# Optimization experiments

Measured on AMD Instinct MI355X. Metric: run time of the kernel, lower is better.

Reference implementation:

```python
import jax, jax.numpy as jnp
import numpy as np

B, T, S, E, H = 64, 256, 512, 128, 512


def setup_inputs() -> dict:
    key = jax.random.key(0)
    ks = jax.random.split(key, 18)
    sc = 0.02
    return {
        "trg_embed": jax.random.normal(ks[0], (B, T, E), jnp.float32),
        "encoder_hidden": jax.random.normal(ks[1], (B, S, 2 * H), jnp.float32),
        "encoder_final_h": jax.random.normal(ks[2], (1, B, 2 * H), jnp.float32),
        "encoder_final_c": jax.random.normal(ks[3], (1, B, 2 * H), jnp.float32),
        "src_mask": jnp.ones((B, 1, S), jnp.bool_),
        "trg_mask": jnp.ones((B, 1, T), jnp.bool_),
        "W_key": jax.random.normal(ks[4], (H, 2 * H), jnp.float32) * sc,
        "W_query": jax.random.normal(ks[5], (H, H), jnp.float32) * sc,
        "v_att": jax.random.normal(ks[6], (H,), jnp.float32) * sc,
        "bridgeh_w": jax.random.normal(ks[7], (H, 2 * H), jnp.float32) * sc,
        "bridgeh_b": jax.random.normal(ks[8], (H,), jnp.float32) * sc,
        "bridgec_w": jax.random.normal(ks[9], (H, 2 * H), jnp.float32) * sc,
        "bridgec_b": jax.random.normal(ks[10], (H,), jnp.float32) * sc,
        "W_ih": jax.random.normal(ks[11], (4 * H, E + 2 * H), jnp.float32) * sc,
        "W_hh": jax.random.normal(ks[12], (4 * H, H), jnp.float32) * sc,
        "b_ih": jax.random.normal(ks[13], (4 * H,), jnp.float32) * sc,
        "b_hh": jax.random.normal(ks[14], (4 * H,), jnp.float32) * sc,
        "W_pre": jax.random.normal(ks[15], (H, H + 2 * H + E), jnp.float32) * sc,
    }


def reference(trg_embed, encoder_hidden, encoder_final_h, encoder_final_c,
              src_mask, trg_mask, W_key, W_query, v_att,
              bridgeh_w, bridgeh_b, bridgec_w, bridgec_b,
              W_ih, W_hh, b_ih, b_hh, W_pre):
    # bridge: init hidden/cell from encoder final states (num_layers=1)
    h = jnp.tanh(encoder_final_h[0] @ bridgeh_w.T + bridgeh_b)  # [B,H]
    c = jnp.tanh(encoder_final_c[0] @ bridgec_w.T + bridgec_b)  # [B,H]

    # Bahdanau attention: precompute key projection once
    proj_key = jnp.einsum('bsk,hk->bsh', encoder_hidden, W_key)  # [B,S,H]
    mask = src_mask[:, 0, :]  # [B,S]
    neg = jnp.asarray(-1e9, encoder_hidden.dtype)

    def step(carry, x_t):
        h, c = carry  # [B,H] each; x_t: [B,E]
        q = h @ W_query.T  # query = last-layer hidden, [B,H]
        scores = jnp.einsum('bsh,h->bs', jnp.tanh(proj_key + q[:, None, :]), v_att)
        scores = jnp.where(mask, scores, neg)
        alphas = jax.nn.softmax(scores, axis=-1)
        ctx = jnp.einsum('bs,bsk->bk', alphas, encoder_hidden)  # [B,2H]
        x = jnp.concatenate([x_t, ctx], axis=-1)  # [B,E+2H]
        gates = x @ W_ih.T + h @ W_hh.T + (b_ih + b_hh)  # [B,4H]
        i, f, g, o = jnp.split(gates, 4, axis=-1)  # torch LSTM gate order
        c_new = jax.nn.sigmoid(f) * c + jax.nn.sigmoid(i) * jnp.tanh(g)
        h_new = jax.nn.sigmoid(o) * jnp.tanh(c_new)
        return (h_new, c_new), (h_new, ctx)

    (h, c), (outs, ctxs) = jax.lax.scan(step, (h, c), jnp.swapaxes(trg_embed, 0, 1))
    outs = jnp.swapaxes(outs, 0, 1)  # decoder_states [B,T,H]
    ctxs = jnp.swapaxes(ctxs, 0, 1)  # [B,T,2H]
    # pre_output projection (dropout p=0 -> identity), batched over all steps
    pre = jnp.concatenate([trg_embed, outs, ctxs], axis=-1) @ W_pre.T  # [B,T,H]
    return outs, h[None], c[None], pre
```

## Files before the change

kernel.cpp:

```cpp
#include <hip/hip_runtime.h>

#define Tq 256
#define Sq 512
#define Hq 512
#define H2q 1024
#define KPACK 1664

typedef __attribute__((ext_vector_type(8))) short short8_t;
typedef __attribute__((ext_vector_type(4))) float f32x4;

__device__ __forceinline__ float bf2f(ushort u){ return __uint_as_float(((unsigned)u)<<16); }
__device__ __forceinline__ ushort f2bf(float f){
  unsigned u = __float_as_uint(f);
  u += 0x7FFFu + ((u>>16)&1u);
  return (ushort)(u>>16);
}
__device__ __forceinline__ float frcp(float x){ return __builtin_amdgcn_rcpf(x); }
__device__ __forceinline__ float fexp2(float x){ return __builtin_amdgcn_exp2f(x); }
__device__ __forceinline__ float ftanh(float x){
  return 1.f - 2.f*frcp(fexp2(2.8853900818f*x) + 1.f);
}
__device__ __forceinline__ float fsig(float x){
  return frcp(1.f + fexp2(-1.4426950409f*x));
}

__global__ void bail_kernel(float* out, float v){
  if (threadIdx.x < 256) out[threadIdx.x] = v;
}

__global__ void conv_bf16(const float* __restrict__ src, ushort* __restrict__ dst, int n4){
  int idx = blockIdx.x*blockDim.x + threadIdx.x;
  if (idx >= n4) return;
  float4 v = ((const float4*)src)[idx];
  ushort4 o; o.x = f2bf(v.x); o.y = f2bf(v.y); o.z = f2bf(v.z); o.w = f2bf(v.w);
  ((ushort4*)dst)[idx] = o;
}

__global__ void conv_fp8(const float* __restrict__ src, unsigned* __restrict__ dst, int n4){
  int idx = blockIdx.x*blockDim.x + threadIdx.x;
  if (idx >= n4) return;
  float4 v = ((const float4*)src)[idx];
  unsigned u = __builtin_amdgcn_cvt_pk_fp8_f32(v.x, v.y, 0u, false);
  u = __builtin_amdgcn_cvt_pk_fp8_f32(v.z, v.w, u, true);
  dst[idx] = u;
}

__global__ void pack_trg(const float* __restrict__ trg, ushort* __restrict__ packed, int n4){
  int idx = blockIdx.x*blockDim.x + threadIdx.x;
  if (idx >= n4) return;
  float4 v = ((const float4*)trg)[idx];
  int bt = idx >> 5, r = idx & 31;
  ushort4 o; o.x = f2bf(v.x); o.y = f2bf(v.y); o.z = f2bf(v.z); o.w = f2bf(v.w);
  *(ushort4*)&packed[(long)bt*KPACK + r*4] = o;
}

__global__ void bsum_kernel(const float* __restrict__ a, const float* __restrict__ b,
                            float* __restrict__ o, int n){
  int idx = blockIdx.x*blockDim.x + threadIdx.x;
  if (idx < n) o[idx] = a[idx] + b[idx];
}

__global__ __launch_bounds__(512)
void bridge_kernel(const float* __restrict__ efh, const float* __restrict__ efc,
                   const float* __restrict__ bhw, const float* __restrict__ bhb,
                   const float* __restrict__ bcw, const float* __restrict__ bcb,
                   float* __restrict__ hb0, float* __restrict__ cws)
{
  int b = blockIdx.x, n = threadIdx.x;
  __shared__ __align__(16) float eh_l[1024];
  __shared__ __align__(16) float ec_l[1024];
  eh_l[n]       = efh[b*1024 + n];
  eh_l[n + 512] = efh[b*1024 + 512 + n];
  ec_l[n]       = efc[b*1024 + n];
  ec_l[n + 512] = efc[b*1024 + 512 + n];
  __syncthreads();
  const float4* wh = (const float4*)(bhw + (long)n*1024);
  const float4* wc = (const float4*)(bcw + (long)n*1024);
  float ah = bhb[n], ac = bcb[n];
  for (int i = 0; i < 256; ++i) {
    float4 w1 = wh[i]; float4 w2 = wc[i];
    const float* e1 = &eh_l[i*4]; const float* e2 = &ec_l[i*4];
    ah += w1.x*e1[0] + w1.y*e1[1] + w1.z*e1[2] + w1.w*e1[3];
    ac += w2.x*e2[0] + w2.y*e2[1] + w2.z*e2[2] + w2.w*e2[3];
  }
  hb0[b*512 + n] = ftanh(ah);
  cws[b*512 + n] = ftanh(ac);
}

__global__ __launch_bounds__(256)
void gemm_bt(const ushort* __restrict__ A, int lda, long sA,
             const ushort* __restrict__ Bt, int ldb, long sB,
             void* __restrict__ Cout, int ldc, long sC, int K, int outMode)
{
  __shared__ __align__(16) ushort Al[128][40];
  __shared__ __align__(16) ushort Bl[128][40];
  int bz = blockIdx.z;
  const ushort* Ab = A + (long)bz*sA;
  const ushort* Bb = Bt + (long)bz*sB;
  int m0 = blockIdx.x*128, n0 = blockIdx.y*128;
  int tid = threadIdx.x;
  int lane = tid & 63, w = tid >> 6;
  int wm = w >> 1, wn = w & 1;
  f32x4 acc[4][4] = {};
  int frow = lane & 15, fk = (lane >> 4)*8;
  for (int k0 = 0; k0 < K; k0 += 32) {
    #pragma unroll
    for (int p = 0; p < 2; ++p) {
      int task = tid + p*256;
      int row = task >> 2, c8 = (task & 3)*8;
      uint4 va = *(const uint4*)(Ab + (long)(m0+row)*lda + k0 + c8);
      uint4 vb = *(const uint4*)(Bb + (long)(n0+row)*ldb + k0 + c8);
      *(uint4*)&Al[row][c8] = va;
      *(uint4*)&Bl[row][c8] = vb;
    }
    __syncthreads();
    short8_t af[4], bfr[4];
    #pragma unroll
    for (int mi = 0; mi < 4; ++mi) af[mi]  = *(const short8_t*)&Al[wm*64 + mi*16 + frow][fk];
    #pragma unroll
    for (int ni = 0; ni < 4; ++ni) bfr[ni] = *(const short8_t*)&Bl[wn*64 + ni*16 + frow][fk];
    #pragma unroll
    for (int mi = 0; mi < 4; ++mi)
      #pragma unroll
      for (int ni = 0; ni < 4; ++ni)
        acc[mi][ni] = __builtin_amdgcn_mfma_f32_16x16x32_bf16(af[mi], bfr[ni], acc[mi][ni], 0, 0, 0);
    __syncthreads();
  }
  int rbase = (lane >> 4)*4;
  int col = lane & 15;
  #pragma unroll
  for (int mi = 0; mi < 4; ++mi)
    #pragma unroll
    for (int ni = 0; ni < 4; ++ni)
      #pragma unroll
      for (int i = 0; i < 4; ++i) {
        int gm = m0 + wm*64 + mi*16 + rbase + i;
        int gn = n0 + wn*64 + ni*16 + col;
        float vv = acc[mi][ni][i];
        long off = (long)bz*sC + (long)gm*ldc + gn;
        if (outMode == 1)      ((ushort*)Cout)[off] = f2bf(vv);
        else if (outMode == 2) ((unsigned char*)Cout)[off] =
              (unsigned char)(__builtin_amdgcn_cvt_pk_fp8_f32(vv, 0.f, 0, false) & 0xFF);
        else                   ((float*)Cout)[off] = vv;
      }
}

__global__ __launch_bounds__(512)
void qstep(const ushort* __restrict__ Wq, const float* __restrict__ hr,
           float* __restrict__ qbuf)
{
  __shared__ __align__(16) float h_s[512];
  int b = blockIdx.x, tid = threadIdx.x;
  h_s[tid] = hr[b*Hq + tid];
  __syncthreads();
  const ushort* wrow = Wq + (long)tid*Hq;
  float qa = 0.f;
  #pragma unroll 4
  for (int k = 0; k < 512; k += 8) {
    uint4 w4 = *(const uint4*)(wrow + k);
    const ushort* wu = (const ushort*)&w4;
    #pragma unroll
    for (int e = 0; e < 8; ++e) qa += h_s[k+e]*bf2f(wu[e]);
  }
  qbuf[b*Hq + tid] = qa;
}

__global__ __launch_bounds__(512)
void scoreA(const unsigned char* __restrict__ pk8,
            const unsigned char* __restrict__ eh8,
            const ushort* __restrict__ qpart,
            const float* __restrict__ qbuf,
            const float* __restrict__ vatt,
            float* __restrict__ ctxp,
            float* __restrict__ denp,
            int useQbuf)
{
  __shared__ __align__(16) float q_s[512];
  __shared__ __align__(16) float v_s[512];
  __shared__ __align__(16) float sred[512];
  __shared__ __align__(16) float e_s[64];
  int tid = threadIdx.x, blk = blockIdx.x;
  int b = blk >> 3, j8 = blk & 7, s0 = j8*64;
  if (useQbuf) {
    q_s[tid] = qbuf[b*Hq + tid];
  } else {
    const ushort* qp = qpart + (long)b*32*512 + tid;
    float qa = 0.f;
    #pragma unroll 8
    for (int c = 0; c < 32; ++c) qa += bf2f(qp[c*512]);
    q_s[tid] = qa;
  }
  v_s[tid] = vatt[tid];
  __syncthreads();
  int sl = tid & 63, hq = tid >> 6;
  {
    const unsigned char* pr = pk8 + ((long)b*Sq + s0 + sl)*Hq + hq*64;
    float p = 0.f;
    #pragma unroll
    for (int i = 0; i < 4; ++i) {
      uint4 w4 = *(const uint4*)(pr + i*16);
      const unsigned* uw = (const unsigned*)&w4;
      #pragma unroll
      for (int m = 0; m < 4; ++m) {
        unsigned u = uw[m];
        int hb = hq*64 + i*16 + m*4;
        p += v_s[hb+0]*ftanh(__builtin_amdgcn_cvt_f32_fp8(u,0) + q_s[hb+0]);
        p += v_s[hb+1]*ftanh(__builtin_amdgcn_cvt_f32_fp8(u,1) + q_s[hb+1]);
        p += v_s[hb+2]*ftanh(__builtin_amdgcn_cvt_f32_fp8(u,2) + q_s[hb+2]);
        p += v_s[hb+3]*ftanh(__builtin_amdgcn_cvt_f32_fp8(u,3) + q_s[hb+3]);
      }
    }
    sred[hq*64 + sl] = p;
  }
  __syncthreads();
  if (tid < 64) {
    float sc = 0.f;
    #pragma unroll
    for (int g = 0; g < 8; ++g) sc += sred[g*64 + tid];
    float e = fexp2(1.4426950409f*sc);
    e_s[tid] = e;
    float r = e;
    #pragma unroll
    for (int off = 32; off; off >>= 1) r += __shfl_down(r, off);
    if (tid == 0) denp[b*8 + j8] = r;
  }
  __syncthreads();
  {
    const unsigned char* ep = eh8 + ((long)b*Sq + s0)*H2q + tid*2;
    float a0 = 0.f, a1 = 0.f;
    #pragma unroll 4
    for (int s = 0; s < 64; ++s) {
      unsigned u = (unsigned)(*(const ushort*)(ep + (long)s*H2q));
      float es = e_s[s];
      a0 += es*__builtin_amdgcn_cvt_f32_fp8(u,0);
      a1 += es*__builtin_amdgcn_cvt_f32_fp8(u,1);
    }
    float* cp = ctxp + ((long)b*8 + j8)*1024 + tid*2;
    cp[0] = a0; cp[1] = a1;
  }
}

__global__ __launch_bounds__(512)
void gatesB(int t, ushort* packed,
            const ushort* __restrict__ Wih, const ushort* __restrict__ Whh,
            const ushort* __restrict__ Wq,
            const float* __restrict__ bsum, const float* __restrict__ hr,
            float* __restrict__ hw, float* __restrict__ cws,
            const float* __restrict__ ctxp, const float* __restrict__ denp,
            ushort* __restrict__ qpart,
            float* __restrict__ outs)
{
  __shared__ __align__(16) float x_lds[8*KPACK];
  __shared__ __align__(16) float g_lds[512];
  __shared__ __align__(16) float rden[8];
  __shared__ __align__(16) float hn_s[128];
  float* redc = x_lds;
  int tid = threadIdx.x, blk = blockIdx.x;
  int c_bg = blk >> 5, c_rc = blk & 31;

  if (tid < 8) {
    int gb = c_bg*8 + tid;
    float d = 0.f;
    #pragma unroll
    for (int j = 0; j < 8; ++j) d += denp[gb*8 + j];
    rden[tid] = frcp(d);
  }
  for (int task = tid; task < 128; task += 512) {
    int bb = task >> 4, c8 = task & 15;
    int gb = c_bg*8 + bb;
    uint4 vv = *(const uint4*)(packed + (long)(gb*Tq + t)*KPACK + c8*8);
    const ushort* uu = (const ushort*)&vv;
    #pragma unroll
    for (int e = 0; e < 8; ++e) x_lds[bb*KPACK + c8*8 + e] = bf2f(uu[e]);
  }
  for (int task = tid; task < 4096; task += 512) {
    int bb = task >> 9, kk = task & 511;
    x_lds[bb*KPACK + 1152 + kk] = hr[(c_bg*8 + bb)*Hq + kk];
  }
  __syncthreads();
  for (int task = tid; task < 8192; task += 512) {
    int bb = task >> 10, kk = task & 1023;
    int gb = c_bg*8 + bb;
    const float* cp = ctxp + (long)gb*8*1024 + kk;
    float cv = 0.f;
    #pragma unroll
    for (int j = 0; j < 8; ++j) cv += cp[j*1024];
    cv *= rden[bb];
    x_lds[bb*KPACK + 128 + kk] = cv;
    if (c_rc == 0) packed[(long)(gb*Tq + t)*KPACK + 640 + kk] = f2bf(cv);
  }
  __syncthreads();
  float acc0[8] = {}, acc1[8] = {};
  int rt = tid & 31, ks = tid >> 5;
  int rowslot0 = rt*2;
  int rr0 = (rowslot0 >> 4)*512 + c_rc*16 + (rowslot0 & 15);
  for (int kt = 0; kt < 13; ++kt) {
    const ushort* w0 = (kt < 9) ? (Wih + (long)rr0*1152 + kt*128 + ks*8)
                                : (Whh + (long)rr0*512  + (kt-9)*128 + ks*8);
    const ushort* w1 = w0 + ((kt < 9) ? 1152 : 512);
    uint4 wa = *(const uint4*)w0;
    uint4 wb = *(const uint4*)w1;
    const ushort* wua = (const ushort*)&wa;
    const ushort* wub = (const ushort*)&wb;
    float wf0[8], wf1[8];
    #pragma unroll
    for (int e = 0; e < 8; ++e) { wf0[e] = bf2f(wua[e]); wf1[e] = bf2f(wub[e]); }
    int xbase = kt*128 + ks*8;
    #pragma unroll
    for (int bb = 0; bb < 8; ++bb) {
      const float* xp = &x_lds[bb*KPACK + xbase];
      float4 x0 = *(const float4*)xp;
      float4 x1 = *(const float4*)(xp + 4);
      acc0[bb] += wf0[0]*x0.x + wf0[1]*x0.y + wf0[2]*x0.z + wf0[3]*x0.w
                + wf0[4]*x1.x + wf0[5]*x1.y + wf0[6]*x1.z + wf0[7]*x1.w;
      acc1[bb] += wf1[0]*x0.x + wf1[1]*x0.y + wf1[2]*x0.z + wf1[3]*x0.w
                + wf1[4]*x1.x + wf1[5]*x1.y + wf1[6]*x1.z + wf1[7]*x1.w;
    }
  }
  __syncthreads();
  #pragma unroll
  for (int bb = 0; bb < 8; ++bb) {
    redc[bb*1024 + ks*64 + rowslot0]     = acc0[bb];
    redc[bb*1024 + ks*64 + rowslot0 + 1] = acc1[bb];
  }
  __syncthreads();
  {
    int rowslot = tid & 63, bb = tid >> 6;
    float gvv = bsum[(rowslot >> 4)*512 + c_rc*16 + (rowslot & 15)];
    #pragma unroll
    for (int q2 = 0; q2 < 16; ++q2) gvv += redc[bb*1024 + q2*64 + rowslot];
    g_lds[bb*64 + rowslot] = gvv;
  }
  __syncthreads();
  if (tid < 128) {
    int bb = tid >> 4, i2 = tid & 15;
    int gb = c_bg*8 + bb;
    int hd = c_rc*16 + i2;
    float gi = g_lds[bb*64 +  0 + i2];
    float gf = g_lds[bb*64 + 16 + i2];
    float gg = g_lds[bb*64 + 32 + i2];
    float go = g_lds[bb*64 + 48 + i2];
    float co = cws[gb*Hq + hd];
    float cn = fsig(gf)*co + fsig(gi)*ftanh(gg);
    float hn = fsig(go)*ftanh(cn);
    cws[gb*Hq + hd] = cn;
    hw[gb*Hq + hd] = hn;
    outs[(long)(gb*Tq + t)*Hq + hd] = hn;
    packed[(long)(gb*Tq + t)*KPACK + 128 + hd] = f2bf(hn);
    hn_s[bb*16 + i2] = hn;
  }
  __syncthreads();
  {
    const ushort* wr = Wq + (long)tid*Hq + c_rc*16;
    uint4 wa = *(const uint4*)wr;
    uint4 wb = *(const uint4*)(wr + 8);
    const ushort* wua = (const ushort*)&wa;
    const ushort* wub = (const ushort*)&wb;
    float wf[16];
    #pragma unroll
    for (int e = 0; e < 8; ++e) { wf[e] = bf2f(wua[e]); wf[8+e] = bf2f(wub[e]); }
    #pragma unroll
    for (int bb = 0; bb < 8; ++bb) {
      const float* hp = &hn_s[bb*16];
      float qa = 0.f;
      #pragma unroll
      for (int e = 0; e < 16; ++e) qa += wf[e]*hp[e];
      qpart[((long)(c_bg*8 + bb)*32 + c_rc)*512 + tid] = f2bf(qa);
    }
  }
}

__global__ void epilogue_copy(const float* __restrict__ hb0, const float* __restrict__ cws,
                              float* __restrict__ dout){
  int idx = blockIdx.x*blockDim.x + threadIdx.x;
  if (idx < 32768) {
    dout[8388608 + idx] = hb0[idx];
    dout[8421376 + idx] = cws[idx];
  }
}

extern "C" void kernel_launch(void* const* d_in, const int* in_sizes, int n_in,
                              void* d_out, int out_size, void* d_ws, size_t ws_size,
                              hipStream_t stream)
{
  float* out = (float*)d_out;
  static const int expect[18] = {2097152,33554432,65536,65536,32768,16384,
                                 524288,262144,512,524288,512,524288,512,
                                 2359296,1048576,2048,2048,851968};
  if (n_in != 18 || out_size != 16842752) {
    bail_kernel<<<1, 256, 0, stream>>>(out, 33.0f); return;
  }
  for (int i = 0; i < 18; ++i) if (in_sizes[i] != expect[i]) {
    bail_kernel<<<1, 256, 0, stream>>>(out, 100.0f + i); return;
  }
  if (ws_size < 166207552ULL) { bail_kernel<<<1, 256, 0, stream>>>(out, 77.0f); return; }

  const float* trg  = (const float*)d_in[0];
  const float* eh   = (const float*)d_in[1];
  const float* efh  = (const float*)d_in[2];
  const float* efc  = (const float*)d_in[3];
  const float* Wk   = (const float*)d_in[6];
  const float* Wq   = (const float*)d_in[7];
  const float* v    = (const float*)d_in[8];
  const float* bhw  = (const float*)d_in[9];
  const float* bhb  = (const float*)d_in[10];
  const float* bcw  = (const float*)d_in[11];
  const float* bcb  = (const float*)d_in[12];
  const float* Wih  = (const float*)d_in[13];
  const float* Whh  = (const float*)d_in[14];
  const float* bih  = (const float*)d_in[15];
  const float* bhh  = (const float*)d_in[16];
  const float* Wpre = (const float*)d_in[17];
  char* ws = (char*)d_ws;

  ushort* ehb          = (ushort*)(ws + 0);
  unsigned char* eh8   = (unsigned char*)(ws + 0);
  unsigned char* pk8   = (unsigned char*)(ws + 67108864);
  ushort* packed       = (ushort*)(ws + 83886080);
  ushort* Wk_b         = (ushort*)(ws + 138412032);
  ushort* Wq_b         = (ushort*)(ws + 139460608);
  ushort* Wih_b        = (ushort*)(ws + 139984896);
  ushort* Whh_b        = (ushort*)(ws + 144703488);
  ushort* Wpre_b       = (ushort*)(ws + 146800640);
  float*  qbuf         = (float*)(ws + 148504576);
  float*  ctxp         = (float*)(ws + 148635648);
  float*  denp         = (float*)(ws + 150732800);
  float*  bsum         = (float*)(ws + 150734848);
  float*  hb0          = (float*)(ws + 150743040);
  float*  hb1          = (float*)(ws + 150874112);
  float*  cws          = (float*)(ws + 151005184);
  ushort* qpart        = (ushort*)(ws + 151136256);

  auto cb = [&](const float* s, ushort* d, int n){
    int n4 = n/4;
    conv_bf16<<<(n4 + 255)/256, 256, 0, stream>>>(s, d, n4);
  };
  cb(eh,   ehb,   64*512*1024);
  cb(Wk,   Wk_b,  512*1024);
  cb(Wq,   Wq_b,  512*512);
  cb(Wih,  Wih_b, 2048*1152);
  cb(Whh,  Whh_b, 2048*512);
  cb(Wpre, Wpre_b,512*1664);
  pack_trg<<<(524288 + 255)/256, 256, 0, stream>>>(trg, packed, 524288);
  bsum_kernel<<<8, 256, 0, stream>>>(bih, bhh, bsum, 2048);
  bridge_kernel<<<64, 512, 0, stream>>>(efh, efc, bhw, bhb, bcw, bcb, hb0, cws);
  gemm_bt<<<dim3(4,4,64), 256, 0, stream>>>(ehb, 1024, 524288L, Wk_b, 1024, 0L,
                                            (void*)pk8, 512, 262144L, 1024, 2);
  conv_fp8<<<(8388608 + 255)/256, 256, 0, stream>>>(eh, (unsigned*)eh8, 8388608);
  qstep<<<64, 512, 0, stream>>>(Wq_b, hb0, qbuf);

  for (int t = 0; t < 256; ++t) {
    const float* hr = (t & 1) ? hb1 : hb0;
    float*       hw = (t & 1) ? hb0 : hb1;
    scoreA<<<512, 512, 0, stream>>>(pk8, eh8, qpart, qbuf, v, ctxp, denp, (t == 0) ? 1 : 0);
    gatesB<<<256, 512, 0, stream>>>(t, packed, Wih_b, Whh_b, Wq_b, bsum, hr, hw, cws,
                                    ctxp, denp, qpart, out);
  }

  epilogue_copy<<<128, 256, 0, stream>>>(hb0, cws, out);
  gemm_bt<<<dim3(128,4,1), 256, 0, stream>>>(packed, 1664, 0L, Wpre_b, 1664, 0L,
                                             (void*)(out + 8454144), 512, 0L, 1664, 0);
}
```

Before: 9.126 ms.

## Compute LSTM gate GEMV with bf16 MFMA and bf16 LDS activations

```diff
diff --git a/kernel.cpp b/kernel.cpp
--- a/kernel.cpp
+++ b/kernel.cpp
@@ -250,13 +250,14 @@
             ushort* __restrict__ qpart,
             float* __restrict__ outs)
 {
-  __shared__ __align__(16) float x_lds[8*KPACK];
-  __shared__ __align__(16) float g_lds[512];
-  __shared__ __align__(16) float rden[8];
-  __shared__ __align__(16) float hn_s[128];
-  float* redc = x_lds;
+  __shared__ __align__(16) ushort x_l[8*1672];
+  __shared__ __align__(16) float  redc[2048];
+  __shared__ __align__(16) float  g_lds[512];
+  __shared__ __align__(16) float  rden[8];
+  __shared__ __align__(16) float  hn_s[128];
   int tid = threadIdx.x, blk = blockIdx.x;
   int c_bg = blk >> 5, c_rc = blk & 31;
+  int lane = tid & 63, wv = tid >> 6;
 
   if (tid < 8) {
     int gb = c_bg*8 + tid;
@@ -269,67 +270,54 @@
     int bb = task >> 4, c8 = task & 15;
     int gb = c_bg*8 + bb;
     uint4 vv = *(const uint4*)(packed + (long)(gb*Tq + t)*KPACK + c8*8);
-    const ushort* uu = (const ushort*)&vv;
-    #pragma unroll
-    for (int e = 0; e < 8; ++e) x_lds[bb*KPACK + c8*8 + e] = bf2f(uu[e]);
+    *(uint4*)&x_l[bb*1672 + c8*8] = vv;
   }
   for (int task = tid; task < 4096; task += 512) {
     int bb = task >> 9, kk = task & 511;
-    x_lds[bb*KPACK + 1152 + kk] = hr[(c_bg*8 + bb)*Hq + kk];
+    x_l[bb*1672 + 1152 + kk] = f2bf(hr[(c_bg*8 + bb)*Hq + kk]);
   }
   __syncthreads();
   for (int task = tid; task < 8192; task += 512) {
     int bb = task >> 10, kk = task & 1023;
     int gb = c_bg*8 + bb;
-    const float* cp = ctxp + (long)gb*8*1024 + kk;
+    const float* cp = ctxp + (long)gb*8192 + kk;
     float cv = 0.f;
     #pragma unroll
     for (int j = 0; j < 8; ++j) cv += cp[j*1024];
     cv *= rden[bb];
-    x_lds[bb*KPACK + 128 + kk] = cv;
-    if (c_rc == 0) packed[(long)(gb*Tq + t)*KPACK + 640 + kk] = f2bf(cv);
-  }
-  __syncthreads();
-  float acc0[8] = {}, acc1[8] = {};
-  int rt = tid & 31, ks = tid >> 5;
-  int rowslot0 = rt*2;
-  int rr0 = (rowslot0 >> 4)*512 + c_rc*16 + (rowslot0 & 15);
-  for (int kt = 0; kt < 13; ++kt) {
-    const ushort* w0 = (kt < 9) ? (Wih + (long)rr0*1152 + kt*128 + ks*8)
-                                : (Whh + (long)rr0*512  + (kt-9)*128 + ks*8);
-    const ushort* w1 = w0 + ((kt < 9) ? 1152 : 512);
-    uint4 wa = *(const uint4*)w0;
-    uint4 wb = *(const uint4*)w1;
-    const ushort* wua = (const ushort*)&wa;
-    const ushort* wub = (const ushort*)&wb;
-    float wf0[8], wf1[8];
-    #pragma unroll
-    for (int e = 0; e < 8; ++e) { wf0[e] = bf2f(wua[e]); wf1[e] = bf2f(wub[e]); }
-    int xbase = kt*128 + ks*8;
-    #pragma unroll
-    for (int bb = 0; bb < 8; ++bb) {
-      const float* xp = &x_lds[bb*KPACK + xbase];
-      float4 x0 = *(const float4*)xp;
-      float4 x1 = *(const float4*)(xp + 4);
-      acc0[bb] += wf0[0]*x0.x + wf0[1]*x0.y + wf0[2]*x0.z + wf0[3]*x0.w
-                + wf0[4]*x1.x + wf0[5]*x1.y + wf0[6]*x1.z + wf0[7]*x1.w;
-      acc1[bb] += wf1[0]*x0.x + wf1[1]*x0.y + wf1[2]*x0.z + wf1[3]*x0.w
-                + wf1[4]*x1.x + wf1[5]*x1.y + wf1[6]*x1.z + wf1[7]*x1.w;
+    ushort cb = f2bf(cv);
+    x_l[bb*1672 + 128 + kk] = cb;
+    if (c_rc == 0) packed[(long)(gb*Tq + t)*KPACK + 640 + kk] = cb;
+  }
+  __syncthreads();
+  {
+    int mt = wv & 3, kh = wv >> 2;
+    f32x4 acc = {};
+    int frow = lane & 15, fk8 = (lane >> 4)*8;
+    int rr = mt*512 + c_rc*16 + frow;
+    const ushort* bp = &x_l[(lane & 7)*1672];
+    #pragma unroll 2
+    for (int i = 0; i < 26; ++i) {
+      int k = (kh*26 + i)*32 + fk8;
+      const ushort* ap = (k < 1152) ? (Wih + (long)rr*1152 + k)
+                                    : (Whh + (long)rr*512 + (k - 1152));
+      short8_t af = *(const short8_t*)ap;
+      short8_t bf = *(const short8_t*)(bp + (k < 1152 ? k : k));
+      acc = __builtin_amdgcn_mfma_f32_16x16x32_bf16(af, bf, acc, 0, 0, 0);
     }
-  }
-  __syncthreads();
-  #pragma unroll
-  for (int bb = 0; bb < 8; ++bb) {
-    redc[bb*1024 + ks*64 + rowslot0]     = acc0[bb];
-    redc[bb*1024 + ks*64 + rowslot0 + 1] = acc1[bb];
+    int crow = (lane >> 4)*4, ccol = lane & 15;
+    #pragma unroll
+    for (int i = 0; i < 4; ++i)
+      redc[((mt*2 + kh)*16 + crow + i)*16 + ccol] = acc[i];
   }
   __syncthreads();
   {
-    int rowslot = tid & 63, bb = tid >> 6;
-    float gvv = bsum[(rowslot >> 4)*512 + c_rc*16 + (rowslot & 15)];
-    #pragma unroll
-    for (int q2 = 0; q2 < 16; ++q2) gvv += redc[bb*1024 + q2*64 + rowslot];
-    g_lds[bb*64 + rowslot] = gvv;
+    int b = tid & 7, lr = tid >> 3;
+    int mt2 = lr >> 4, mrow = lr & 15;
+    float g = bsum[mt2*512 + c_rc*16 + mrow]
+            + redc[((mt2*2 + 0)*16 + mrow)*16 + b]
+            + redc[((mt2*2 + 1)*16 + mrow)*16 + b];
+    g_lds[b*64 + lr] = g;
   }
   __syncthreads();
   if (tid < 128) {
```

New measurement: 9.861 ms. 1.08x slower.

## Fold tanh scaling into key projection and store gate inputs as bf16 in LDS

Applied to the files above, without the earlier changes.

```diff
diff --git a/kernel.cpp b/kernel.cpp
--- a/kernel.cpp
+++ b/kernel.cpp
@@ -58,6 +58,22 @@
                             float* __restrict__ o, int n){
   int idx = blockIdx.x*blockDim.x + threadIdx.x;
   if (idx < n) o[idx] = a[idx] + b[idx];
+}
+
+__global__ void vsum_kernel(const float* __restrict__ v, float* __restrict__ o){
+  __shared__ float red[8];
+  int tid = threadIdx.x;
+  float x = v[tid];
+  #pragma unroll
+  for (int off = 32; off; off >>= 1) x += __shfl_down(x, off);
+  if ((tid & 63) == 0) red[tid >> 6] = x;
+  __syncthreads();
+  if (tid == 0) {
+    float s = 0.f;
+    #pragma unroll
+    for (int i = 0; i < 8; ++i) s += red[i];
+    o[0] = s;
+  }
 }
 
 __global__ __launch_bounds__(512)
@@ -90,7 +106,8 @@
 __global__ __launch_bounds__(256)
 void gemm_bt(const ushort* __restrict__ A, int lda, long sA,
              const ushort* __restrict__ Bt, int ldb, long sB,
-             void* __restrict__ Cout, int ldc, long sC, int K, int outMode)
+             void* __restrict__ Cout, int ldc, long sC, int K, int outMode,
+             float oscale)
 {
   __shared__ __align__(16) ushort Al[128][40];
   __shared__ __align__(16) ushort Bl[128][40];
@@ -140,7 +157,7 @@
         long off = (long)bz*sC + (long)gm*ldc + gn;
         if (outMode == 1)      ((ushort*)Cout)[off] = f2bf(vv);
         else if (outMode == 2) ((unsigned char*)Cout)[off] =
-              (unsigned char)(__builtin_amdgcn_cvt_pk_fp8_f32(vv, 0.f, 0, false) & 0xFF);
+              (unsigned char)(__builtin_amdgcn_cvt_pk_fp8_f32(vv*oscale, 0.f, 0, false) & 0xFF);
         else                   ((float*)Cout)[off] = vv;
       }
 }
@@ -171,26 +188,29 @@
             const ushort* __restrict__ qpart,
             const float* __restrict__ qbuf,
             const float* __restrict__ vatt,
+            const float* __restrict__ vsumb,
             float* __restrict__ ctxp,
             float* __restrict__ denp,
             int useQbuf)
 {
   __shared__ __align__(16) float q_s[512];
-  __shared__ __align__(16) float v_s[512];
+  __shared__ __align__(16) float v2_s[512];
   __shared__ __align__(16) float sred[512];
   __shared__ __align__(16) float e_s[64];
   int tid = threadIdx.x, blk = blockIdx.x;
   int b = blk >> 3, j8 = blk & 7, s0 = j8*64;
+  float qraw;
   if (useQbuf) {
-    q_s[tid] = qbuf[b*Hq + tid];
+    qraw = qbuf[b*Hq + tid];
   } else {
     const ushort* qp = qpart + (long)b*32*512 + tid;
     float qa = 0.f;
     #pragma unroll 8
     for (int c = 0; c < 32; ++c) qa += bf2f(qp[c*512]);
-    q_s[tid] = qa;
-  }
-  v_s[tid] = vatt[tid];
+    qraw = qa;
+  }
+  q_s[tid] = 2.8853900818f*qraw;
+  v2_s[tid] = -2.f*vatt[tid];
   __syncthreads();
   int sl = tid & 63, hq = tid >> 6;
   {
@@ -204,17 +224,17 @@
       for (int m = 0; m < 4; ++m) {
         unsigned u = uw[m];
         int hb = hq*64 + i*16 + m*4;
-        p += v_s[hb+0]*ftanh(__builtin_amdgcn_cvt_f32_fp8(u,0) + q_s[hb+0]);
-        p += v_s[hb+1]*ftanh(__builtin_amdgcn_cvt_f32_fp8(u,1) + q_s[hb+1]);
-        p += v_s[hb+2]*ftanh(__builtin_amdgcn_cvt_f32_fp8(u,2) + q_s[hb+2]);
-        p += v_s[hb+3]*ftanh(__builtin_amdgcn_cvt_f32_fp8(u,3) + q_s[hb+3]);
+        p += v2_s[hb+0]*frcp(fexp2(__builtin_amdgcn_cvt_f32_fp8(u,0) + q_s[hb+0]) + 1.f);
+        p += v2_s[hb+1]*frcp(fexp2(__builtin_amdgcn_cvt_f32_fp8(u,1) + q_s[hb+1]) + 1.f);
+        p += v2_s[hb+2]*frcp(fexp2(__builtin_amdgcn_cvt_f32_fp8(u,2) + q_s[hb+2]) + 1.f);
+        p += v2_s[hb+3]*frcp(fexp2(__builtin_amdgcn_cvt_f32_fp8(u,3) + q_s[hb+3]) + 1.f);
       }
     }
     sred[hq*64 + sl] = p;
   }
   __syncthreads();
   if (tid < 64) {
-    float sc = 0.f;
+    float sc = vsumb[0];
     #pragma unroll
     for (int g = 0; g < 8; ++g) sc += sred[g*64 + tid];
     float e = fexp2(1.4426950409f*sc);
@@ -250,11 +270,11 @@
             ushort* __restrict__ qpart,
             float* __restrict__ outs)
 {
-  __shared__ __align__(16) float x_lds[8*KPACK];
-  __shared__ __align__(16) float g_lds[512];
-  __shared__ __align__(16) float rden[8];
-  __shared__ __align__(16) float hn_s[128];
-  float* redc = x_lds;
+  __shared__ __align__(16) ushort x_l[8*1672];
+  __shared__ __align__(16) float  redc[8192];
+  __shared__ __align__(16) float  g_lds[512];
+  __shared__ __align__(16) float  rden[8];
+  __shared__ __align__(16) float  hn_s[128];
   int tid = threadIdx.x, blk = blockIdx.x;
   int c_bg = blk >> 5, c_rc = blk & 31;
 
@@ -269,25 +289,24 @@
     int bb = task >> 4, c8 = task & 15;
     int gb = c_bg*8 + bb;
     uint4 vv = *(const uint4*)(packed + (long)(gb*Tq + t)*KPACK + c8*8);
-    const ushort* uu = (const ushort*)&vv;
-    #pragma unroll
-    for (int e = 0; e < 8; ++e) x_lds[bb*KPACK + c8*8 + e] = bf2f(uu[e]);
+    *(uint4*)&x_l[bb*1672 + c8*8] = vv;
   }
   for (int task = tid; task < 4096; task += 512) {
     int bb = task >> 9, kk = task & 511;
-    x_lds[bb*KPACK + 1152 + kk] = hr[(c_bg*8 + bb)*Hq + kk];
+    x_l[bb*1672 + 1152 + kk] = f2bf(hr[(c_bg*8 + bb)*Hq + kk]);
   }
   __syncthreads();
   for (int task = tid; task < 8192; task += 512) {
     int bb = task >> 10, kk = task & 1023;
     int gb = c_bg*8 + bb;
-    const float* cp = ctxp + (long)gb*8*1024 + kk;
+    const float* cp = ctxp + (long)gb*8192 + kk;
     float cv = 0.f;
     #pragma unroll
     for (int j = 0; j < 8; ++j) cv += cp[j*1024];
     cv *= rden[bb];
-    x_lds[bb*KPACK + 128 + kk] = cv;
-    if (c_rc == 0) packed[(long)(gb*Tq + t)*KPACK + 640 + kk] = f2bf(cv);
+    ushort cb = f2bf(cv);
+    x_l[bb*1672 + 128 + kk] = cb;
+    if (c_rc == 0) packed[(long)(gb*Tq + t)*KPACK + 640 + kk] = cb;
   }
   __syncthreads();
   float acc0[8] = {}, acc1[8] = {};
@@ -308,13 +327,15 @@
     int xbase = kt*128 + ks*8;
     #pragma unroll
     for (int bb = 0; bb < 8; ++bb) {
-      const float* xp = &x_lds[bb*KPACK + xbase];
-      float4 x0 = *(const float4*)xp;
-      float4 x1 = *(const float4*)(xp + 4);
-      acc0[bb] += wf0[0]*x0.x + wf0[1]*x0.y + wf0[2]*x0.z + wf0[3]*x0.w
-                + wf0[4]*x1.x + wf0[5]*x1.y + wf0[6]*x1.z + wf0[7]*x1.w;
-      acc1[bb] += wf1[0]*x0.x + wf1[1]*x0.y + wf1[2]*x0.z + wf1[3]*x0.w
-                + wf1[4]*x1.x + wf1[5]*x1.y + wf1[6]*x1.z + wf1[7]*x1.w;
+      uint4 uv = *(const uint4*)&x_l[bb*1672 + xbase];
+      float x0 = __uint_as_float(uv.x << 16), x1 = __uint_as_float(uv.x & 0xFFFF0000u);
+      float x2 = __uint_as_float(uv.y << 16), x3 = __uint_as_float(uv.y & 0xFFFF0000u);
+      float x4 = __uint_as_float(uv.z << 16), x5 = __uint_as_float(uv.z & 0xFFFF0000u);
+      float x6 = __uint_as_float(uv.w << 16), x7 = __uint_as_float(uv.w & 0xFFFF0000u);
+      acc0[bb] += wf0[0]*x0 + wf0[1]*x1 + wf0[2]*x2 + wf0[3]*x3
+                + wf0[4]*x4 + wf0[5]*x5 + wf0[6]*x6 + wf0[7]*x7;
+      acc1[bb] += wf1[0]*x0 + wf1[1]*x1 + wf1[2]*x2 + wf1[3]*x3
+                + wf1[4]*x4 + wf1[5]*x5 + wf1[6]*x6 + wf1[7]*x7;
     }
   }
   __syncthreads();
@@ -430,6 +451,7 @@
   float*  hb1          = (float*)(ws + 150874112);
   float*  cws          = (float*)(ws + 151005184);
   ushort* qpart        = (ushort*)(ws + 151136256);
+  float*  vsumb        = (float*)(ws + 153233408);
 
   auto cb = [&](const float* s, ushort* d, int n){
     int n4 = n/4;
@@ -443,21 +465,23 @@
   cb(Wpre, Wpre_b,512*1664);
   pack_trg<<<(524288 + 255)/256, 256, 0, stream>>>(trg, packed, 524288);
   bsum_kernel<<<8, 256, 0, stream>>>(bih, bhh, bsum, 2048);
+  vsum_kernel<<<1, 512, 0, stream>>>(v, vsumb);
   bridge_kernel<<<64, 512, 0, stream>>>(efh, efc, bhw, bhb, bcw, bcb, hb0, cws);
   gemm_bt<<<dim3(4,4,64), 256, 0, stream>>>(ehb, 1024, 524288L, Wk_b, 1024, 0L,
-                                            (void*)pk8, 512, 262144L, 1024, 2);
+                                            (void*)pk8, 512, 262144L, 1024, 2, 2.8853900818f);
   conv_fp8<<<(8388608 + 255)/256, 256, 0, stream>>>(eh, (unsigned*)eh8, 8388608);
   qstep<<<64, 512, 0, stream>>>(Wq_b, hb0, qbuf);
 
   for (int t = 0; t < 256; ++t) {
     const float* hr = (t & 1) ? hb1 : hb0;
     float*       hw = (t & 1) ? hb0 : hb1;
-    scoreA<<<512, 512, 0, stream>>>(pk8, eh8, qpart, qbuf, v, ctxp, denp, (t == 0) ? 1 : 0);
+    scoreA<<<512, 512, 0, stream>>>(pk8, eh8, qpart, qbuf, v, vsumb, ctxp, denp,
+                                    (t == 0) ? 1 : 0);
     gatesB<<<256, 512, 0, stream>>>(t, packed, Wih_b, Whh_b, Wq_b, bsum, hr, hw, cws,
                                     ctxp, denp, qpart, out);
   }
 
   epilogue_copy<<<128, 256, 0, stream>>>(hb0, cws, out);
   gemm_bt<<<dim3(128,4,1), 256, 0, stream>>>(packed, 1664, 0L, Wpre_b, 1664, 0L,
-                                             (void*)(out + 8454144), 512, 0L, 1664, 0);
-}
+                                             (void*)(out + 8454144), 512, 0L, 1664, 0, 1.f);
+}
```

New measurement: 10.13 ms. +11.0%, slower.
